# Kernel tuning notes

Hardware: AMD Instinct MI355X
Metric: run time of the kernel (lower is better)

## Reference

```python
import jax, jax.numpy as jnp
import numpy as np

DIM = 512
NUM_HEADS = 16
HEAD_DIM = DIM // NUM_HEADS
HIDDEN = int(DIM * 4.0)
EPS = 1e-5


def layer_norm(x, gamma, beta):
    mu = jnp.mean(x, axis=-1, keepdims=True)
    var = jnp.mean(jnp.square(x - mu), axis=-1, keepdims=True)
    return (x - mu) * jax.lax.rsqrt(var + EPS) * gamma + beta


def setup_inputs() -> dict:
    key = jax.random.key(0)
    ks = jax.random.split(key, 8)
    B, L, C = 32, 3136, DIM
    x = jax.random.normal(ks[0], (B, L, C), dtype=jnp.float32)
    norm1_g = jnp.ones((C,), jnp.float32)
    norm1_b = jnp.zeros((C,), jnp.float32)
    # spatial (per-head) mixing weight: (num_heads, head_dim, head_dim)
    w_spatial = jax.random.normal(ks[1], (NUM_HEADS, HEAD_DIM, HEAD_DIM), jnp.float32) * (1.0 / np.sqrt(HEAD_DIM))
    norm2_g = jnp.ones((C,), jnp.float32)
    norm2_b = jnp.zeros((C,), jnp.float32)
    w1 = jax.random.normal(ks[2], (C, HIDDEN), jnp.float32) * (1.0 / np.sqrt(C))
    b1 = jnp.zeros((HIDDEN,), jnp.float32)
    w2 = jax.random.normal(ks[3], (HIDDEN, C), jnp.float32) * (1.0 / np.sqrt(HIDDEN))
    b2 = jnp.zeros((C,), jnp.float32)
    return {"x": x, "norm1_g": norm1_g, "norm1_b": norm1_b, "w_spatial": w_spatial,
            "norm2_g": norm2_g, "norm2_b": norm2_b, "w1": w1, "b1": b1, "w2": w2, "b2": b2}


def reference(x, norm1_g, norm1_b, w_spatial, norm2_g, norm2_b, w1, b1, w2, b2):
    B, L, C = x.shape
    shortcut = x
    h = layer_norm(x, norm1_g, norm1_b)
    # window partition -> per-head channel-sub-dim linear (shared across windows/positions)
    # mathematically equivalent to applying the per-head matmul at every token
    h = h.reshape(B, L, NUM_HEADS, HEAD_DIM)
    h = jnp.einsum('blhd,hde->blhe', h, w_spatial)
    h = h.reshape(B, L, C)
    x = shortcut + h
    # channel MLP: Linear -> GELU(tanh) -> Linear
    y = layer_norm(x, norm2_g, norm2_b)
    y = jax.nn.gelu(y @ w1 + b1, approximate=True)
    y = y @ w2 + b2
    return x + y
```

## Files before the change

kernel.cpp:

```cpp
#include <hip/hip_runtime.h>
#include <hip/hip_bf16.h>


typedef __bf16 bf16x8 __attribute__((ext_vector_type(8)));
typedef float f32x4 __attribute__((ext_vector_type(4)));

constexpr int CDIM = 512;
constexpr int HID = 2048;
constexpr int MROWS = 32 * 3136;
constexpr float LN_EPS = 1e-5f;

static __device__ __forceinline__ float gelu_tanh(float x) {
  const float u = 0.7978845608028654f * fmaf(0.044715f * x * x, x, x);
  const float e = __expf(2.0f * u);
  return 0.5f * x * (2.0f - 2.0f / (e + 1.0f));
}

static __device__ __forceinline__ void load_lds16(const void* g, void* l) {
  __builtin_amdgcn_global_load_lds((__attribute__((address_space(1))) void*)g,
                                   (__attribute__((address_space(3))) void*)l,
                                   16, 0, 0);
}

template <int KD>
__global__ __launch_bounds__(256) void cvt_t(const float* __restrict__ src,
                                             __hip_bfloat16* __restrict__ dst,
                                             int ND) {
  const int i = blockIdx.x * 256 + threadIdx.x;
  const int n = i / KD;
  const int k = i - n * KD;
  dst[i] = __float2bfloat16(src[(size_t)k * ND + n]);
}

__global__ __launch_bounds__(256) void fused_pre(
    const float* __restrict__ x, const float* __restrict__ g1,
    const float* __restrict__ b1, const float* __restrict__ wsp,
    const float* __restrict__ g2, const float* __restrict__ b2,
    float* __restrict__ x2out, __hip_bfloat16* __restrict__ yout) {
  __shared__ float lnbuf[CDIM];
  __shared__ float red[8];

  const int t = threadIdx.x;
  const int lane = t & 63;
  const int w = t >> 6;
  const int c0 = t, c1 = t + 256;
  const int hd0 = c0 >> 5, e0 = c0 & 31;
  const int hd1 = c1 >> 5, e1 = c1 & 31;

  float wc0[32], wc1[32];
#pragma unroll
  for (int d = 0; d < 32; ++d) {
    wc0[d] = wsp[(hd0 * 32 + d) * 32 + e0];
    wc1[d] = wsp[(hd1 * 32 + d) * 32 + e1];
  }
  const float g1v0 = g1[c0], g1v1 = g1[c1], b1v0 = b1[c0], b1v1 = b1[c1];
  const float g2v0 = g2[c0], g2v1 = g2[c1], b2v0 = b2[c0], b2v1 = b2[c1];

  for (int r = blockIdx.x; r < MROWS; r += gridDim.x) {
    const float* xr = x + (size_t)r * CDIM;
    const float xv0 = xr[c0], xv1 = xr[c1];

    float s = xv0 + xv1, ss = xv0 * xv0 + xv1 * xv1;
#pragma unroll
    for (int off = 32; off; off >>= 1) {
      s += __shfl_down(s, off);
      ss += __shfl_down(ss, off);
    }
    if (lane == 0) { red[w * 2] = s; red[w * 2 + 1] = ss; }
    __syncthreads();
    s = red[0] + red[2] + red[4] + red[6];
    ss = red[1] + red[3] + red[5] + red[7];
    float mu = s * (1.0f / CDIM);
    float var = ss * (1.0f / CDIM) - mu * mu;
    float rs = rsqrtf(var + LN_EPS);
    lnbuf[c0] = (xv0 - mu) * rs * g1v0 + b1v0;
    lnbuf[c1] = (xv1 - mu) * rs * g1v1 + b1v1;
    __syncthreads();

    float h0 = 0.f, h1 = 0.f;
#pragma unroll
    for (int d = 0; d < 32; ++d) {
      h0 = fmaf(lnbuf[hd0 * 32 + d], wc0[d], h0);
      h1 = fmaf(lnbuf[hd1 * 32 + d], wc1[d], h1);
    }
    const float a0 = xv0 + h0, a1 = xv1 + h1;
    x2out[(size_t)r * CDIM + c0] = a0;
    x2out[(size_t)r * CDIM + c1] = a1;

    s = a0 + a1;
    ss = a0 * a0 + a1 * a1;
#pragma unroll
    for (int off = 32; off; off >>= 1) {
      s += __shfl_down(s, off);
      ss += __shfl_down(ss, off);
    }
    if (lane == 0) { red[w * 2] = s; red[w * 2 + 1] = ss; }
    __syncthreads();
    s = red[0] + red[2] + red[4] + red[6];
    ss = red[1] + red[3] + red[5] + red[7];
    mu = s * (1.0f / CDIM);
    var = ss * (1.0f / CDIM) - mu * mu;
    rs = rsqrtf(var + LN_EPS);
    yout[(size_t)r * CDIM + c0] = __float2bfloat16((a0 - mu) * rs * g2v0 + b2v0);
    yout[(size_t)r * CDIM + c1] = __float2bfloat16((a1 - mu) * rs * g2v1 + b2v1);
    __syncthreads();
  }
}

template <int K, int N, bool GELU>
__global__ __launch_bounds__(512, 2) void gemm8p(
    const __hip_bfloat16* __restrict__ A, const __hip_bfloat16* __restrict__ Bt,
    const float* __restrict__ bias, __hip_bfloat16* __restrict__ zout,
    float* __restrict__ fout) {
  constexpr int NT = N / 256;
  constexpr int NKT = K / 32;
  __shared__ __attribute__((aligned(16))) __hip_bfloat16 lds[4][2][256 * 32];

  const int tid = threadIdx.x;
  const int lane = tid & 63;
  const int w = tid >> 6;
  const int wm = w >> 2, wn = w & 3;

  const int cpx = gridDim.x >> 3;
  const int bid = (blockIdx.x & 7) * cpx + (blockIdx.x >> 3);
  const int tm = bid / NT, tn = bid - tm * NT;
  const size_t am0 = (size_t)tm * 256;
  const int bn0 = tn * 256;

  const int r0 = tid >> 2;
  const int ks0 = (tid & 3) ^ ((tid >> 2) & 3) ^ ((tid >> 4) & 3);
  const __hip_bfloat16* aP0 = A + (am0 + r0) * K + ks0 * 8;
  const __hip_bfloat16* aP1 = aP0 + (size_t)128 * K;
  const __hip_bfloat16* bP0 = Bt + (size_t)(bn0 + r0) * K + ks0 * 8;
  const __hip_bfloat16* bP1 = bP0 + (size_t)128 * K;
  const int lo0 = (w * 64) * 8;
  const int lo1 = (512 + w * 64) * 8;

#define STAGE_A(sl, kt)                            \
  do {                                             \
    load_lds16(aP0 + (kt) * 32, &lds[sl][0][lo0]); \
    load_lds16(aP1 + (kt) * 32, &lds[sl][0][lo1]); \
  } while (0)
#define STAGE_B(sl, kt)                            \
  do {                                             \
    load_lds16(bP0 + (kt) * 32, &lds[sl][1][lo0]); \
    load_lds16(bP1 + (kt) * 32, &lds[sl][1][lo1]); \
  } while (0)

  f32x4 acc[8][4] = {};
  const int fr = lane & 15;
  const int kgs = (((lane >> 4) ^ (lane & 3) ^ ((lane >> 2) & 3))) * 8;

  STAGE_A(0, 0);
  STAGE_B(0, 0);
  STAGE_A(1, 1);
  STAGE_B(1, 1);

  for (int t = 0; t < NKT; ++t) {
    if (t + 1 < NKT)
      asm volatile("s_waitcnt vmcnt(4)" ::: "memory");
    else
      asm volatile("s_waitcnt vmcnt(0)" ::: "memory");
    __builtin_amdgcn_s_barrier();

    const int sl = t & 3;
    const int s2 = (t + 2) & 3;
    const bool pf = (t + 2) < NKT;
    const __hip_bfloat16* As = lds[sl][0];
    const __hip_bfloat16* Bs = lds[sl][1];

    if (pf) STAGE_A(s2, t + 2);
    bf16x8 bfv[4];
#pragma unroll
    for (int n = 0; n < 4; ++n)
      bfv[n] = *(const bf16x8*)(Bs + (wn * 64 + n * 16 + fr) * 32 + kgs);
    bf16x8 af[4];
#pragma unroll
    for (int m = 0; m < 4; ++m)
      af[m] = *(const bf16x8*)(As + (wm * 128 + m * 16 + fr) * 32 + kgs);
    __builtin_amdgcn_s_setprio(1);
#pragma unroll
    for (int m = 0; m < 4; ++m)
#pragma unroll
      for (int n = 0; n < 4; ++n)
        acc[m][n] = __builtin_amdgcn_mfma_f32_16x16x32_bf16(af[m], bfv[n],
                                                            acc[m][n], 0, 0, 0);
    __builtin_amdgcn_s_setprio(0);
    __builtin_amdgcn_s_barrier();

    if (pf) STAGE_B(s2, t + 2);
#pragma unroll
    for (int m = 0; m < 4; ++m)
      af[m] = *(const bf16x8*)(As + (wm * 128 + (m + 4) * 16 + fr) * 32 + kgs);
    __builtin_amdgcn_s_setprio(1);
#pragma unroll
    for (int m = 0; m < 4; ++m)
#pragma unroll
      for (int n = 0; n < 4; ++n)
        acc[m + 4][n] = __builtin_amdgcn_mfma_f32_16x16x32_bf16(
            af[m], bfv[n], acc[m + 4][n], 0, 0, 0);
    __builtin_amdgcn_s_setprio(0);
  }
#undef STAGE_A
#undef STAGE_B

  const int cr = (lane >> 4) * 4;
  const int cc = lane & 15;
#pragma unroll
  for (int n = 0; n < 4; ++n) {
    const int col = bn0 + wn * 64 + n * 16 + cc;
    const float bv = bias[col];
#pragma unroll
    for (int m = 0; m < 8; ++m) {
      const size_t row = am0 + wm * 128 + m * 16 + cr;
#pragma unroll
      for (int j = 0; j < 4; ++j) {
        const float v = acc[m][n][j] + bv;
        const size_t off = (row + j) * N + col;
        if constexpr (GELU) {
          zout[off] = __float2bfloat16(gelu_tanh(v));
        } else {
          fout[off] = fout[off] + v;
        }
      }
    }
  }
}

extern "C" void kernel_launch(void* const* d_in, const int* in_sizes, int n_in,
                              void* d_out, int out_size, void* d_ws,
                              size_t ws_size, hipStream_t stream) {
  const float* x = (const float*)d_in[0];
  const float* n1g = (const float*)d_in[1];
  const float* n1b = (const float*)d_in[2];
  const float* wsp = (const float*)d_in[3];
  const float* n2g = (const float*)d_in[4];
  const float* n2b = (const float*)d_in[5];
  const float* w1 = (const float*)d_in[6];
  const float* b1 = (const float*)d_in[7];
  const float* w2 = (const float*)d_in[8];
  const float* b2 = (const float*)d_in[9];
  float* out = (float*)d_out;

  __hip_bfloat16* ybuf = (__hip_bfloat16*)d_ws;
  __hip_bfloat16* zbuf = ybuf + (size_t)MROWS * CDIM;
  __hip_bfloat16* w1t = zbuf + (size_t)MROWS * HID;
  __hip_bfloat16* w2t = w1t + (size_t)CDIM * HID;

  cvt_t<CDIM><<<(CDIM * HID) / 256, 256, 0, stream>>>(w1, w1t, HID);
  cvt_t<HID><<<(CDIM * HID) / 256, 256, 0, stream>>>(w2, w2t, CDIM);
  fused_pre<<<2048, 256, 0, stream>>>(x, n1g, n1b, wsp, n2g, n2b, out, ybuf);
  gemm8p<CDIM, HID, true><<<(MROWS / 256) * (HID / 256), 512, 0, stream>>>(
      ybuf, w1t, b1, zbuf, nullptr);
  gemm8p<HID, CDIM, false><<<(MROWS / 256) * (CDIM / 256), 512, 0, stream>>>(
      zbuf, w2t, b2, nullptr, out);
}
```

Measured before the change: 939.3 us.

## Restructure GEMM pipeline with K=64 double buffer, LDS-staged epilogue, vectorized prepass

The GEMM main loop now walks K in steps of 64 with a two-deep double buffer of two 32-wide halves. It uses a new rotate-style LDS swizzle and interleaves staging loads, LDS fragment loads and MFMA bursts with explicit barriers and waitcnts. The epilogue stages results through LDS so global stores are coalesced 16-byte writes: bf16 for the GELU output, and float4 read-modify-write for the residual add. The prepass kernel switches to float2/bf16x2 accesses with two adjacent channels per thread. The aim is better load/compute overlap and fewer uncoalesced epilogue stores, at the cost of more barriers per K step.

```diff
diff --git a/kernel.cpp b/kernel.cpp
--- a/kernel.cpp
+++ b/kernel.cpp
@@ -43,24 +43,25 @@
   const int t = threadIdx.x;
   const int lane = t & 63;
   const int w = t >> 6;
-  const int c0 = t, c1 = t + 256;
-  const int hd0 = c0 >> 5, e0 = c0 & 31;
-  const int hd1 = c1 >> 5, e1 = c1 & 31;
+  const int c0 = 2 * t;
+  const int hd = c0 >> 5, e0 = c0 & 31;
 
   float wc0[32], wc1[32];
 #pragma unroll
   for (int d = 0; d < 32; ++d) {
-    wc0[d] = wsp[(hd0 * 32 + d) * 32 + e0];
-    wc1[d] = wsp[(hd1 * 32 + d) * 32 + e1];
+    const float2 wv = *(const float2*)&wsp[(hd * 32 + d) * 32 + e0];
+    wc0[d] = wv.x;
+    wc1[d] = wv.y;
   }
-  const float g1v0 = g1[c0], g1v1 = g1[c1], b1v0 = b1[c0], b1v1 = b1[c1];
-  const float g2v0 = g2[c0], g2v1 = g2[c1], b2v0 = b2[c0], b2v1 = b2[c1];
+  const float2 g1v = *(const float2*)&g1[c0];
+  const float2 b1v = *(const float2*)&b1[c0];
+  const float2 g2v = *(const float2*)&g2[c0];
+  const float2 b2v = *(const float2*)&b2[c0];
 
   for (int r = blockIdx.x; r < MROWS; r += gridDim.x) {
-    const float* xr = x + (size_t)r * CDIM;
-    const float xv0 = xr[c0], xv1 = xr[c1];
-
-    float s = xv0 + xv1, ss = xv0 * xv0 + xv1 * xv1;
+    const float2 xv = *(const float2*)&x[(size_t)r * CDIM + c0];
+
+    float s = xv.x + xv.y, ss = xv.x * xv.x + xv.y * xv.y;
 #pragma unroll
     for (int off = 32; off; off >>= 1) {
       s += __shfl_down(s, off);
@@ -73,19 +74,22 @@
     float mu = s * (1.0f / CDIM);
     float var = ss * (1.0f / CDIM) - mu * mu;
     float rs = rsqrtf(var + LN_EPS);
-    lnbuf[c0] = (xv0 - mu) * rs * g1v0 + b1v0;
-    lnbuf[c1] = (xv1 - mu) * rs * g1v1 + b1v1;
+    lnbuf[c0] = (xv.x - mu) * rs * g1v.x + b1v.x;
+    lnbuf[c0 + 1] = (xv.y - mu) * rs * g1v.y + b1v.y;
     __syncthreads();
 
     float h0 = 0.f, h1 = 0.f;
 #pragma unroll
     for (int d = 0; d < 32; ++d) {
-      h0 = fmaf(lnbuf[hd0 * 32 + d], wc0[d], h0);
-      h1 = fmaf(lnbuf[hd1 * 32 + d], wc1[d], h1);
-    }
-    const float a0 = xv0 + h0, a1 = xv1 + h1;
-    x2out[(size_t)r * CDIM + c0] = a0;
-    x2out[(size_t)r * CDIM + c1] = a1;
+      const float lv = lnbuf[hd * 32 + d];
+      h0 = fmaf(lv, wc0[d], h0);
+      h1 = fmaf(lv, wc1[d], h1);
+    }
+    const float a0 = xv.x + h0, a1 = xv.y + h1;
+    float2 av;
+    av.x = a0;
+    av.y = a1;
+    *(float2*)&x2out[(size_t)r * CDIM + c0] = av;
 
     s = a0 + a1;
     ss = a0 * a0 + a1 * a1;
@@ -101,20 +105,22 @@
     mu = s * (1.0f / CDIM);
     var = ss * (1.0f / CDIM) - mu * mu;
     rs = rsqrtf(var + LN_EPS);
-    yout[(size_t)r * CDIM + c0] = __float2bfloat16((a0 - mu) * rs * g2v0 + b2v0);
-    yout[(size_t)r * CDIM + c1] = __float2bfloat16((a1 - mu) * rs * g2v1 + b2v1);
+    __hip_bfloat162 yv;
+    yv.x = __float2bfloat16((a0 - mu) * rs * g2v.x + b2v.x);
+    yv.y = __float2bfloat16((a1 - mu) * rs * g2v.y + b2v.y);
+    *(__hip_bfloat162*)&yout[(size_t)r * CDIM + c0] = yv;
     __syncthreads();
   }
 }
 
 template <int K, int N, bool GELU>
-__global__ __launch_bounds__(512, 2) void gemm8p(
+__global__ __launch_bounds__(512, 2) void gemm4p(
     const __hip_bfloat16* __restrict__ A, const __hip_bfloat16* __restrict__ Bt,
     const float* __restrict__ bias, __hip_bfloat16* __restrict__ zout,
     float* __restrict__ fout) {
   constexpr int NT = N / 256;
-  constexpr int NKT = K / 32;
-  __shared__ __attribute__((aligned(16))) __hip_bfloat16 lds[4][2][256 * 32];
+  constexpr int NKT = K / 64;
+  __shared__ __attribute__((aligned(16))) __hip_bfloat16 sm[2][2][2][8192];
 
   const int tid = threadIdx.x;
   const int lane = tid & 63;
@@ -127,101 +133,170 @@
   const size_t am0 = (size_t)tm * 256;
   const int bn0 = tn * 256;
 
-  const int r0 = tid >> 2;
-  const int ks0 = (tid & 3) ^ ((tid >> 2) & 3) ^ ((tid >> 4) & 3);
-  const __hip_bfloat16* aP0 = A + (am0 + r0) * K + ks0 * 8;
-  const __hip_bfloat16* aP1 = aP0 + (size_t)128 * K;
-  const __hip_bfloat16* bP0 = Bt + (size_t)(bn0 + r0) * K + ks0 * 8;
-  const __hip_bfloat16* bP1 = bP0 + (size_t)128 * K;
-  const int lo0 = (w * 64) * 8;
-  const int lo1 = (512 + w * 64) * 8;
-
-#define STAGE_A(sl, kt)                            \
-  do {                                             \
-    load_lds16(aP0 + (kt) * 32, &lds[sl][0][lo0]); \
-    load_lds16(aP1 + (kt) * 32, &lds[sl][0][lo1]); \
-  } while (0)
-#define STAGE_B(sl, kt)                            \
-  do {                                             \
-    load_lds16(bP0 + (kt) * 32, &lds[sl][1][lo0]); \
-    load_lds16(bP1 + (kt) * 32, &lds[sl][1][lo1]); \
-  } while (0)
+  const int srow = tid >> 2;
+  const int kphys = tid & 3;
+  const int sks = (kphys - srow - ((srow >> 2) & 1)) & 3;
+  const __hip_bfloat16* pA0 = A + (am0 + srow) * K + sks * 8;
+  const __hip_bfloat16* pA1 = pA0 + (size_t)128 * K;
+  const __hip_bfloat16* pB0 = Bt + (size_t)(bn0 + srow) * K + sks * 8;
+  const __hip_bfloat16* pB1 = pB0 + (size_t)128 * K;
+  const int off0 = w * 512;
+  const int off1 = 4096 + w * 512;
+
+  const int fr = lane & 15, kg = lane >> 4;
+  const int kls = (kg + fr + ((fr >> 2) & 1)) & 3;
+  const int rbyte = fr * 64 + kls * 16;
 
   f32x4 acc[8][4] = {};
-  const int fr = lane & 15;
-  const int kgs = (((lane >> 4) ^ (lane & 3) ^ ((lane >> 2) & 3))) * 8;
-
-  STAGE_A(0, 0);
-  STAGE_B(0, 0);
-  STAGE_A(1, 1);
-  STAGE_B(1, 1);
+  bf16x8 af[4], bfv[4];
+
+#define STAGE_A(d, s, t)                                       \
+  do {                                                         \
+    load_lds16(pA0 + (t) * 64 + (s) * 32, &sm[d][0][s][off0]); \
+    load_lds16(pA1 + (t) * 64 + (s) * 32, &sm[d][0][s][off1]); \
+  } while (0)
+#define STAGE_B(d, s, t)                                       \
+  do {                                                         \
+    load_lds16(pB0 + (t) * 64 + (s) * 32, &sm[d][1][s][off0]); \
+    load_lds16(pB1 + (t) * 64 + (s) * 32, &sm[d][1][s][off1]); \
+  } while (0)
+#define LOAD_AF(d, s, mh)                                                    \
+  do {                                                                       \
+    _Pragma("unroll") for (int m = 0; m < 4; ++m) af[m] =                    \
+        *(const bf16x8*)((const char*)&sm[d][0][s][0] +                      \
+                         (wm * 128 + (mh)*64 + m * 16) * 64 + rbyte);        \
+  } while (0)
+#define LOAD_BF(d, s)                                                        \
+  do {                                                                       \
+    _Pragma("unroll") for (int n = 0; n < 4; ++n) bfv[n] =                   \
+        *(const bf16x8*)((const char*)&sm[d][1][s][0] + (wn * 64 + n * 16) * \
+                             64 + rbyte);                                    \
+  } while (0)
+#define BAR_LG()                                          \
+  do {                                                    \
+    __builtin_amdgcn_s_barrier();                         \
+    asm volatile("s_waitcnt lgkmcnt(0)" ::: "memory");    \
+    __builtin_amdgcn_sched_barrier(0);                    \
+  } while (0)
+#define MM(mh)                                                            \
+  do {                                                                    \
+    __builtin_amdgcn_s_setprio(1);                                        \
+    _Pragma("unroll") for (int m = 0; m < 4; ++m)                         \
+        _Pragma("unroll") for (int n = 0; n < 4; ++n) acc[(mh)*4 + m][n] =\
+            __builtin_amdgcn_mfma_f32_16x16x32_bf16(af[m], bfv[n],        \
+                                                    acc[(mh)*4 + m][n],   \
+                                                    0, 0, 0);             \
+    __builtin_amdgcn_s_setprio(0);                                        \
+  } while (0)
+
+  STAGE_A(0, 0, 0);
+  STAGE_B(0, 0, 0);
+  STAGE_A(0, 1, 0);
+  STAGE_B(0, 1, 0);
+  STAGE_A(1, 0, 1);
+  STAGE_B(1, 0, 1);
+  asm volatile("s_waitcnt vmcnt(8)" ::: "memory");
+  __builtin_amdgcn_s_barrier();
 
   for (int t = 0; t < NKT; ++t) {
-    if (t + 1 < NKT)
-      asm volatile("s_waitcnt vmcnt(4)" ::: "memory");
+    const int d = t & 1, dn = d ^ 1;
+    const bool st1 = (t + 1) < NKT, st2 = (t + 2) < NKT;
+    LOAD_AF(d, 0, 0);
+    LOAD_BF(d, 0);
+    if (st1) STAGE_A(dn, 1, t + 1);
+    BAR_LG();
+    MM(0);
+    __builtin_amdgcn_s_barrier();
+    LOAD_AF(d, 0, 1);
+    if (st1) STAGE_B(dn, 1, t + 1);
+    BAR_LG();
+    MM(1);
+    if (st1)
+      asm volatile("s_waitcnt vmcnt(8)" ::: "memory");
     else
       asm volatile("s_waitcnt vmcnt(0)" ::: "memory");
     __builtin_amdgcn_s_barrier();
-
-    const int sl = t & 3;
-    const int s2 = (t + 2) & 3;
-    const bool pf = (t + 2) < NKT;
-    const __hip_bfloat16* As = lds[sl][0];
-    const __hip_bfloat16* Bs = lds[sl][1];
-
-    if (pf) STAGE_A(s2, t + 2);
-    bf16x8 bfv[4];
-#pragma unroll
-    for (int n = 0; n < 4; ++n)
-      bfv[n] = *(const bf16x8*)(Bs + (wn * 64 + n * 16 + fr) * 32 + kgs);
-    bf16x8 af[4];
-#pragma unroll
-    for (int m = 0; m < 4; ++m)
-      af[m] = *(const bf16x8*)(As + (wm * 128 + m * 16 + fr) * 32 + kgs);
-    __builtin_amdgcn_s_setprio(1);
-#pragma unroll
-    for (int m = 0; m < 4; ++m)
-#pragma unroll
-      for (int n = 0; n < 4; ++n)
-        acc[m][n] = __builtin_amdgcn_mfma_f32_16x16x32_bf16(af[m], bfv[n],
-                                                            acc[m][n], 0, 0, 0);
-    __builtin_amdgcn_s_setprio(0);
+    LOAD_AF(d, 1, 0);
+    LOAD_BF(d, 1);
+    if (st2) STAGE_A(d, 0, t + 2);
+    BAR_LG();
+    MM(0);
     __builtin_amdgcn_s_barrier();
-
-    if (pf) STAGE_B(s2, t + 2);
-#pragma unroll
-    for (int m = 0; m < 4; ++m)
-      af[m] = *(const bf16x8*)(As + (wm * 128 + (m + 4) * 16 + fr) * 32 + kgs);
-    __builtin_amdgcn_s_setprio(1);
-#pragma unroll
-    for (int m = 0; m < 4; ++m)
-#pragma unroll
-      for (int n = 0; n < 4; ++n)
-        acc[m + 4][n] = __builtin_amdgcn_mfma_f32_16x16x32_bf16(
-            af[m], bfv[n], acc[m + 4][n], 0, 0, 0);
-    __builtin_amdgcn_s_setprio(0);
+    LOAD_AF(d, 1, 1);
+    if (st2) STAGE_B(d, 0, t + 2);
+    BAR_LG();
+    MM(1);
+    if (st2)
+      asm volatile("s_waitcnt vmcnt(8)" ::: "memory");
+    else if (st1)
+      asm volatile("s_waitcnt vmcnt(4)" ::: "memory");
+    __builtin_amdgcn_s_barrier();
   }
 #undef STAGE_A
 #undef STAGE_B
+#undef LOAD_AF
+#undef LOAD_BF
+#undef BAR_LG
+#undef MM
 
   const int cr = (lane >> 4) * 4;
   const int cc = lane & 15;
-#pragma unroll
-  for (int n = 0; n < 4; ++n) {
-    const int col = bn0 + wn * 64 + n * 16 + cc;
-    const float bv = bias[col];
-#pragma unroll
-    for (int m = 0; m < 8; ++m) {
-      const size_t row = am0 + wm * 128 + m * 16 + cr;
-#pragma unroll
-      for (int j = 0; j < 4; ++j) {
-        const float v = acc[m][n][j] + bv;
-        const size_t off = (row + j) * N + col;
-        if constexpr (GELU) {
-          zout[off] = __float2bfloat16(gelu_tanh(v));
-        } else {
-          fout[off] = fout[off] + v;
+  char* smb = (char*)&sm[0][0][0][0];
+
+  if constexpr (GELU) {
+    __hip_bfloat16* ot = (__hip_bfloat16*)smb;
+#pragma unroll
+    for (int n = 0; n < 4; ++n) {
+      const int col = wn * 64 + n * 16 + cc;
+      const float bv = bias[bn0 + col];
+#pragma unroll
+      for (int m = 0; m < 8; ++m) {
+        const int row = wm * 128 + m * 16 + cr;
+#pragma unroll
+        for (int j = 0; j < 4; ++j)
+          ot[(row + j) * 256 + col] = __float2bfloat16(gelu_tanh(acc[m][n][j] + bv));
+      }
+    }
+    __syncthreads();
+#pragma unroll
+    for (int it = 0; it < 16; ++it) {
+      const int seg = it * 512 + tid;
+      const int row = seg >> 5, ch = seg & 31;
+      const uint4 v = *(const uint4*)(smb + seg * 16);
+      *(uint4*)&zout[(am0 + row) * N + bn0 + ch * 8] = v;
+    }
+  } else {
+#pragma unroll
+    for (int p = 0; p < 2; ++p) {
+      if (p) __syncthreads();
+      if (wm == p) {
+        float* ot = (float*)smb;
+#pragma unroll
+        for (int n = 0; n < 4; ++n) {
+          const int col = wn * 64 + n * 16 + cc;
+          const float bv = bias[bn0 + col];
+#pragma unroll
+          for (int m = 0; m < 8; ++m) {
+            const int row = m * 16 + cr;
+#pragma unroll
+            for (int j = 0; j < 4; ++j)
+              ot[(row + j) * 256 + col] = acc[m][n][j] + bv;
+          }
         }
+      }
+      __syncthreads();
+#pragma unroll
+      for (int it = 0; it < 16; ++it) {
+        const int seg = it * 512 + tid;
+        const int row = seg >> 6, ch = seg & 63;
+        const float4 lv = *(const float4*)(smb + seg * 16);
+        float* gp = &fout[(am0 + p * 128 + row) * N + bn0 + ch * 4];
+        float4 o = *(const float4*)gp;
+        o.x += lv.x;
+        o.y += lv.y;
+        o.z += lv.z;
+        o.w += lv.w;
+        *(float4*)gp = o;
       }
     }
   }
@@ -250,8 +325,8 @@
   cvt_t<CDIM><<<(CDIM * HID) / 256, 256, 0, stream>>>(w1, w1t, HID);
   cvt_t<HID><<<(CDIM * HID) / 256, 256, 0, stream>>>(w2, w2t, CDIM);
   fused_pre<<<2048, 256, 0, stream>>>(x, n1g, n1b, wsp, n2g, n2b, out, ybuf);
-  gemm8p<CDIM, HID, true><<<(MROWS / 256) * (HID / 256), 512, 0, stream>>>(
+  gemm4p<CDIM, HID, true><<<(MROWS / 256) * (HID / 256), 512, 0, stream>>>(
       ybuf, w1t, b1, zbuf, nullptr);
-  gemm8p<HID, CDIM, false><<<(MROWS / 256) * (CDIM / 256), 512, 0, stream>>>(
+  gemm4p<HID, CDIM, false><<<(MROWS / 256) * (CDIM / 256), 512, 0, stream>>>(
       zbuf, w2t, b2, nullptr, out);
 }
```

Result: slower. 960.9 us (+2.3%).
